# Kernel optimization log

Measured on AMD Instinct MI355X. Metric: run time of the kernel, lower is better.

The kernel has to match this reference:

```python
import jax, jax.numpy as jnp
import numpy as np

N = 100000   # nodes (single ntype)
R = 3        # relations
E = 500000   # edges per relation
H = 4        # attention heads
F = 64       # out_feat per head
IN = 256     # in_feat
NEG_SLOPE = 0.2  # DGL GATConv default


def setup_inputs() -> dict:
    key = jax.random.key(0)
    ks = jax.random.split(key, 7)
    x = jax.random.normal(ks[0], (N, IN), jnp.float32)
    src = jax.random.randint(ks[1], (R, E), 0, N, dtype=jnp.int32)
    dst = jax.random.randint(ks[2], (R, E), 0, N, dtype=jnp.int32)
    W = jax.random.normal(ks[3], (R, IN, H * F), jnp.float32) / np.sqrt(IN).astype(np.float32)
    attn_l = jax.random.normal(ks[4], (R, H, F), jnp.float32) * 0.1
    attn_r = jax.random.normal(ks[5], (R, H, F), jnp.float32) * 0.1
    bias = jnp.zeros((R, H * F), jnp.float32)
    return {"x": x, "W": W, "attn_l": attn_l, "attn_r": attn_r, "bias": bias,
            "src": src, "dst": dst}


def _gat_relation(x, W_r, al_r, ar_r, b_r, src_r, dst_r):
    # projection: [N, H, F]
    z = (x @ W_r).reshape(N, H, F)
    # per-node attention logits: [N, H]
    el = jnp.sum(z * al_r, axis=-1)
    er = jnp.sum(z * ar_r, axis=-1)
    # edge scores: [E, H]
    e = jax.nn.leaky_relu(el[src_r] + er[dst_r], negative_slope=NEG_SLOPE)
    # segment softmax over incoming edges of each dst node
    m = jax.ops.segment_max(e, dst_r, num_segments=N)      # [N, H]
    ee = jnp.exp(e - m[dst_r])                              # [E, H]
    den = jax.ops.segment_sum(ee, dst_r, num_segments=N)   # [N, H]
    alpha = ee / den[dst_r]                                 # [E, H]
    # weighted scatter-aggregate: [N, H, F]
    rst = jax.ops.segment_sum(z[src_r] * alpha[:, :, None], dst_r, num_segments=N)
    return rst + b_r.reshape(1, H, F)


def reference(x, W, attn_l, attn_r, bias, src, dst):
    # HeteroGraphConv aggregates relations targeting the same ntype with 'sum'
    out = jnp.zeros((N, H, F), x.dtype)
    for r in range(R):
        out = out + _gat_relation(x, W[r], attn_l[r], attn_r[r], bias[r], src[r], dst[r])
    # RelGATConvLayer._apply: activation(h.view(-1, out_feat*num_heads)); dropout=0
    return jax.nn.elu(out.reshape(N, H * F))
```

## Files before the change

### kernel.cpp

```cpp
#include <hip/hip_runtime.h>
#include <hip/hip_bf16.h>


#define RN 100000
#define RE 500000
#define RH 4
#define RIN 256
#define RR 3
#define RHF 256
#define NE3 (RR * RE)
#define N3  (RR * RN)

typedef __attribute__((ext_vector_type(8))) short short8;
typedef __attribute__((ext_vector_type(4))) float f32x4;

static __device__ __forceinline__ float b2f(unsigned short u) {
  return __uint_as_float(((unsigned int)u) << 16);
}
static __device__ __forceinline__ unsigned short f2b(float f) {
  unsigned int u = __float_as_uint(f);
  u += 0x7FFF + ((u >> 16) & 1);
  return (unsigned short)(u >> 16);
}
static __device__ __forceinline__ float h2f(unsigned short u) {
  return (float)__builtin_bit_cast(_Float16, u);
}
static __device__ __forceinline__ unsigned short f2h(float f) {
  return __builtin_bit_cast(unsigned short, (_Float16)f);
}
static __device__ __forceinline__ unsigned int cvt_pk_bf16(float lo, float hi) {
  unsigned int r;
  asm("v_cvt_pk_bf16_f32 %0, %1, %2" : "=v"(r) : "v"(lo), "v"(hi));
  return r;
}

__global__ __launch_bounds__(256) void rgat_convx(
    const float* __restrict__ x, unsigned short* __restrict__ xb) {
  const size_t i = ((size_t)blockIdx.x * 256 + threadIdx.x) * 4;
  if (i >= (size_t)RN * RIN) return;
  const float4 v = *(const float4*)(x + i);
  ushort4 o;
  o.x = f2b(v.x); o.y = f2b(v.y); o.z = f2b(v.z); o.w = f2b(v.w);
  *(ushort4*)(xb + i) = o;
}

__global__ __launch_bounds__(256) void rgat_convw(
    const float* __restrict__ W, unsigned short* __restrict__ wbt) {
  const int o = blockIdx.x * 256 + threadIdx.x;
  if (o >= RR * RIN * RHF) return;
  const int r = o / (RIN * RHF);
  const int rem = o - r * (RIN * RHF);
  const int n = rem >> 8;
  const int k = rem & 255;
  wbt[o] = f2b(W[r * (RIN * RHF) + k * RHF + n]);
}

__global__ __launch_bounds__(256) void rgat_gemm_bf16(
    const unsigned short* __restrict__ xb, const unsigned short* __restrict__ wbt,
    unsigned short* __restrict__ zb, const float* __restrict__ al,
    const float* __restrict__ ar, unsigned short* __restrict__ elh,
    unsigned short* __restrict__ erh) {
  __shared__ unsigned short As[128 * 32];
  __shared__ unsigned short Bs[128 * 32];
  const int tid = threadIdx.x;
  const int lane = tid & 63, wid = tid >> 6;
  const int wr = wid >> 1, wc = wid & 1;
  const int m0 = blockIdx.x * 128;
  const int n0 = blockIdx.y * 128;
  const int r  = blockIdx.z;

  f32x4 acc[4][4] = {};
  const unsigned short* Bbase = wbt + (size_t)r * (RIN * RHF);

  for (int k0 = 0; k0 < RIN; k0 += 32) {
#pragma unroll
    for (int i = 0; i < 2; ++i) {
      const int c = wid * 128 + i * 64 + lane;
      const int row = c >> 2, c4 = c & 3;
      const unsigned short* ga = xb + (size_t)(m0 + row) * RIN + k0 + c4 * 8;
      __builtin_amdgcn_global_load_lds(
          (const __attribute__((address_space(1))) void*)ga,
          (__attribute__((address_space(3))) void*)(As + (wid * 128 + i * 64) * 8),
          16, 0, 0);
      const unsigned short* gb = Bbase + (size_t)(n0 + row) * RIN + k0 + c4 * 8;
      __builtin_amdgcn_global_load_lds(
          (const __attribute__((address_space(1))) void*)gb,
          (__attribute__((address_space(3))) void*)(Bs + (wid * 128 + i * 64) * 8),
          16, 0, 0);
    }
    asm volatile("s_waitcnt vmcnt(0)" ::: "memory");
    __syncthreads();

    short8 wf[4], xf[4];
#pragma unroll
    for (int ci = 0; ci < 4; ++ci)
      wf[ci] = *(const short8*)(Bs + ((wr * 64 + ci * 16 + (lane & 15)) * 32 + (lane >> 4) * 8));
#pragma unroll
    for (int xi = 0; xi < 4; ++xi)
      xf[xi] = *(const short8*)(As + ((wc * 64 + xi * 16 + (lane & 15)) * 32 + (lane >> 4) * 8));
#pragma unroll
    for (int ci = 0; ci < 4; ++ci)
#pragma unroll
      for (int xi = 0; xi < 4; ++xi)
        acc[ci][xi] = __builtin_amdgcn_mfma_f32_16x16x32_bf16(wf[ci], xf[xi], acc[ci][xi], 0, 0, 0);
    __syncthreads();
  }

  const int head = blockIdx.y * 2 + wr;
  const int g4 = (lane >> 4) * 4;
  float alv[4][4], arv[4][4];
#pragma unroll
  for (int ci = 0; ci < 4; ++ci) {
    const float4 a4 = *(const float4*)(al + r * RHF + head * 64 + ci * 16 + g4);
    const float4 b4 = *(const float4*)(ar + r * RHF + head * 64 + ci * 16 + g4);
    alv[ci][0] = a4.x; alv[ci][1] = a4.y; alv[ci][2] = a4.z; alv[ci][3] = a4.w;
    arv[ci][0] = b4.x; arv[ci][1] = b4.y; arv[ci][2] = b4.z; arv[ci][3] = b4.w;
  }

#pragma unroll
  for (int xi = 0; xi < 4; ++xi) {
    const int node = m0 + wc * 64 + xi * 16 + (lane & 15);
    unsigned short* zrow = zb + (size_t)r * ((size_t)RN * RHF) + (size_t)node * RHF
                           + n0 + wr * 64 + g4;
    float pl = 0.f, pr = 0.f;
#pragma unroll
    for (int ci = 0; ci < 4; ++ci) {
      const f32x4 a = acc[ci][xi];
      uint2 pk;
      pk.x = cvt_pk_bf16(a[0], a[1]);
      pk.y = cvt_pk_bf16(a[2], a[3]);
      if (node < RN) *(uint2*)(zrow + ci * 16) = pk;
      pl += a[0] * alv[ci][0] + a[1] * alv[ci][1] + a[2] * alv[ci][2] + a[3] * alv[ci][3];
      pr += a[0] * arv[ci][0] + a[1] * arv[ci][1] + a[2] * arv[ci][2] + a[3] * arv[ci][3];
    }
    pl += __shfl_xor(pl, 16); pl += __shfl_xor(pl, 32);
    pr += __shfl_xor(pr, 16); pr += __shfl_xor(pr, 32);
    if (lane < 16 && node < RN) {
      const size_t key = (size_t)r * RN + node;
      elh[key * RH + head] = f2h(pl);
      erh[key * RH + head] = f2h(pr);
    }
  }
}

__global__ __launch_bounds__(256) void rgat_hist(
    const int* __restrict__ dst, int* __restrict__ deg2) {
  const int i = blockIdx.x * 256 + threadIdx.x;
  if (i >= NE3) return;
  const int r = i / RE;
  atomicAdd(&deg2[dst[i] * RR + r], 1);
}

__global__ __launch_bounds__(256) void rgat_scan1(
    const int* __restrict__ deg, int* __restrict__ offs, int* __restrict__ bsum) {
  __shared__ int sh[256];
  const int tid = threadIdx.x;
  const int base = blockIdx.x * 1024 + tid * 4;
  int v[4]; int s = 0;
#pragma unroll
  for (int j = 0; j < 4; ++j) {
    v[j] = (base + j < N3) ? deg[base + j] : 0;
    s += v[j];
  }
  sh[tid] = s;
  __syncthreads();
  for (int off = 1; off < 256; off <<= 1) {
    int t = (tid >= off) ? sh[tid - off] : 0;
    __syncthreads();
    sh[tid] += t;
    __syncthreads();
  }
  int run = sh[tid] - s;
  if (tid == 255) bsum[blockIdx.x] = sh[255];
#pragma unroll
  for (int j = 0; j < 4; ++j) {
    if (base + j < N3) offs[base + j] = run;
    run += v[j];
  }
}

__global__ __launch_bounds__(512) void rgat_scan2(int* __restrict__ bsum, int nb) {
  __shared__ int sh[512];
  const int tid = threadIdx.x;
  const int v = (tid < nb) ? bsum[tid] : 0;
  sh[tid] = v;
  __syncthreads();
  for (int off = 1; off < 512; off <<= 1) {
    int t = (tid >= off) ? sh[tid - off] : 0;
    __syncthreads();
    sh[tid] += t;
    __syncthreads();
  }
  if (tid < nb) bsum[tid] = sh[tid] - v;
}

__global__ __launch_bounds__(256) void rgat_scan3(
    int* __restrict__ offs, const int* __restrict__ bsum) {
  const int base = blockIdx.x * 1024 + threadIdx.x * 4;
  const int b = bsum[blockIdx.x];
#pragma unroll
  for (int j = 0; j < 4; ++j)
    if (base + j < N3) offs[base + j] += b;
}

__global__ __launch_bounds__(256) void rgat_scatter(
    const int* __restrict__ src, const int* __restrict__ dst,
    const unsigned short* __restrict__ elh, const unsigned short* __restrict__ erh,
    int* __restrict__ offs2, int* __restrict__ czoff,
    unsigned short* __restrict__ ceeh) {
  const int i = blockIdx.x * 256 + threadIdx.x;
  if (i >= NE3) return;
  const int r = i / RE;
  const int s = src[i];
  const int d = dst[i];
  const int pos = atomicAdd(&offs2[d * RR + r], 1);
  const uint2 eu = *(const uint2*)(elh + ((size_t)r * RN + s) * RH);
  const uint2 ru = *(const uint2*)(erh + ((size_t)r * RN + d) * RH);
  float e0 = h2f((unsigned short)eu.x) + h2f((unsigned short)ru.x);
  float e1 = h2f((unsigned short)(eu.x >> 16)) + h2f((unsigned short)(ru.x >> 16));
  float e2 = h2f((unsigned short)eu.y) + h2f((unsigned short)ru.y);
  float e3 = h2f((unsigned short)(eu.y >> 16)) + h2f((unsigned short)(ru.y >> 16));
  e0 = e0 > 0.f ? e0 : 0.2f * e0;
  e1 = e1 > 0.f ? e1 : 0.2f * e1;
  e2 = e2 > 0.f ? e2 : 0.2f * e2;
  e3 = e3 > 0.f ? e3 : 0.2f * e3;
  czoff[pos] = r * RN + s;
  uint2 o;
  o.x = (unsigned int)f2h(__expf(e0)) | ((unsigned int)f2h(__expf(e1)) << 16);
  o.y = (unsigned int)f2h(__expf(e2)) | ((unsigned int)f2h(__expf(e3)) << 16);
  *(uint2*)(ceeh + (size_t)pos * 4) = o;
}

__global__ __launch_bounds__(256) void rgat_norm(
    unsigned short* __restrict__ ceeh, const int* __restrict__ deg2,
    const int* __restrict__ offs2) {
  const int key = blockIdx.x * 256 + threadIdx.x;
  if (key >= N3) return;
  const int d = deg2[key];
  const int end = offs2[key];
  float s0 = 0.f, s1 = 0.f, s2 = 0.f, s3 = 0.f;
  for (int p = end - d; p < end; ++p) {
    const uint2 v = *(const uint2*)(ceeh + (size_t)p * 4);
    s0 += h2f((unsigned short)v.x);
    s1 += h2f((unsigned short)(v.x >> 16));
    s2 += h2f((unsigned short)v.y);
    s3 += h2f((unsigned short)(v.y >> 16));
  }
  const float i0 = s0 > 0.f ? 1.f / s0 : 0.f;
  const float i1 = s1 > 0.f ? 1.f / s1 : 0.f;
  const float i2 = s2 > 0.f ? 1.f / s2 : 0.f;
  const float i3 = s3 > 0.f ? 1.f / s3 : 0.f;
  for (int p = end - d; p < end; ++p) {
    uint2 v = *(const uint2*)(ceeh + (size_t)p * 4);
    const float a0 = h2f((unsigned short)v.x) * i0;
    const float a1 = h2f((unsigned short)(v.x >> 16)) * i1;
    const float a2 = h2f((unsigned short)v.y) * i2;
    const float a3 = h2f((unsigned short)(v.y >> 16)) * i3;
    v.x = (unsigned int)f2h(a0) | ((unsigned int)f2h(a1) << 16);
    v.y = (unsigned int)f2h(a2) | ((unsigned int)f2h(a3) << 16);
    *(uint2*)(ceeh + (size_t)p * 4) = v;
  }
}

__global__ __launch_bounds__(256) void rgat_aggregate(
    const unsigned short* __restrict__ zb, const int* __restrict__ czoff,
    const unsigned short* __restrict__ ceeh, const int* __restrict__ deg2,
    const int* __restrict__ offs2, const float* __restrict__ bias,
    float* __restrict__ out) {
  __shared__ float shn[4][RHF];
  const int n = blockIdx.x;
  const int tid = threadIdx.x;
  const int wid = tid >> 6, lane = tid & 63;
  const int hw = lane >> 5;
  const int sub = lane & 31;
  const int hwid = wid * 2 + hw;
  const int h = sub >> 3;
  const int c = sub * 8;

  const int k0 = n * RR;
  const int start = offs2[k0] - deg2[k0];
  const int dm = offs2[k0 + 2] - start;

  float acc[8] = {};
  const unsigned short* zB = zb + c;

  for (int base = 0; base < dm; base += 16) {
    int ss[2]; float aa[2];
#pragma unroll
    for (int j = 0; j < 2; ++j) {
      const int t = base + j * 8 + hwid;
      const int tc = t < dm ? t : dm - 1;
      const int p = start + tc;
      ss[j] = czoff[p];
      const float af = h2f(ceeh[(size_t)p * 4 + h]);
      aa[j] = t < dm ? af : 0.f;
    }
    short8 zv[2];
#pragma unroll
    for (int j = 0; j < 2; ++j)
      zv[j] = *(const short8*)(zB + (size_t)ss[j] * RHF);
#pragma unroll
    for (int j = 0; j < 2; ++j) {
      const float a = aa[j];
#pragma unroll
      for (int k = 0; k < 8; ++k)
        acc[k] += a * b2f((unsigned short)zv[j][k]);
    }
  }

#pragma unroll
  for (int k = 0; k < 8; ++k) acc[k] += __shfl_xor(acc[k], 32);

  if (lane < 32) {
    *(float4*)&shn[wid][c]     = make_float4(acc[0], acc[1], acc[2], acc[3]);
    *(float4*)&shn[wid][c + 4] = make_float4(acc[4], acc[5], acc[6], acc[7]);
  }
  __syncthreads();

  const int col = tid;
  float v = shn[0][col] + shn[1][col] + shn[2][col] + shn[3][col]
          + bias[col] + bias[RHF + col] + bias[2 * RHF + col];
  v = v > 0.f ? v : (__expf(v) - 1.f);
  out[(size_t)n * RHF + col] = v;
}

extern "C" void kernel_launch(void* const* d_in, const int* in_sizes, int n_in,
                              void* d_out, int out_size, void* d_ws, size_t ws_size,
                              hipStream_t stream) {
  const float* x    = (const float*)d_in[0];
  const float* W    = (const float*)d_in[1];
  const float* al   = (const float*)d_in[2];
  const float* ar   = (const float*)d_in[3];
  const float* bias = (const float*)d_in[4];
  const int*   src  = (const int*)d_in[5];
  const int*   dst  = (const int*)d_in[6];
  float* out = (float*)d_out;

  char* p = (char*)d_ws;
  unsigned short* xb   = (unsigned short*)p; p += (size_t)RN * RIN * 2;
  unsigned short* wbt  = (unsigned short*)p; p += (size_t)RR * RIN * RHF * 2;
  unsigned short* zb   = (unsigned short*)p; p += (size_t)RR * RN * RHF * 2;
  unsigned short* elh  = (unsigned short*)p; p += (size_t)N3 * RH * 2;
  unsigned short* erh  = (unsigned short*)p; p += (size_t)N3 * RH * 2;
  int* deg2    = (int*)p;    p += (size_t)N3 * 4;
  int* offs2   = (int*)p;    p += (size_t)N3 * 4;
  int* czoff   = (int*)p;    p += (size_t)NE3 * 4;
  unsigned short* ceeh = (unsigned short*)p; p += (size_t)NE3 * RH * 2;
  int* bsum    = (int*)p;    p += 2048;

  const int NB1 = (N3 + 1023) / 1024;

  hipMemsetAsync(deg2, 0, (size_t)N3 * 4, stream);

  rgat_convx<<<(RN * RIN / 4 + 255) / 256, 256, 0, stream>>>(x, xb);
  rgat_convw<<<(RR * RIN * RHF + 255) / 256, 256, 0, stream>>>(W, wbt);

  rgat_hist<<<(NE3 + 255) / 256, 256, 0, stream>>>(dst, deg2);
  rgat_scan1<<<NB1, 256, 0, stream>>>(deg2, offs2, bsum);
  rgat_scan2<<<1, 512, 0, stream>>>(bsum, NB1);
  rgat_scan3<<<NB1, 256, 0, stream>>>(offs2, bsum);

  rgat_gemm_bf16<<<dim3((RN + 127) / 128, RHF / 128, RR), 256, 0, stream>>>(
      xb, wbt, zb, al, ar, elh, erh);

  rgat_scatter<<<(NE3 + 255) / 256, 256, 0, stream>>>(src, dst, elh, erh, offs2,
                                                      czoff, ceeh);

  rgat_norm<<<(N3 + 255) / 256, 256, 0, stream>>>(ceeh, deg2, offs2);

  rgat_aggregate<<<RN, 256, 0, stream>>>(zb, czoff, ceeh, deg2, offs2, bias, out);
}
```

Before: 603.5 us.

## Widen GEMM tile to full 256 columns and move edge score computation into norm

The GEMM block now covers all 256 output columns (all four heads) per 128-node tile, so each block loads the x tile once instead of twice. It drops the grid's column dimension, doubles the B shared buffer and per-thread accumulators, which raises register pressure. Edge logit and exp computation moves from the atomic scatter kernel into the per-destination norm kernel. There it reuses the destination's er value and the CSR source offsets, and the sum is taken in fp32 before fp16 rounding, so scatter no longer writes the ceeh buffer.

```diff
diff --git a/kernel.cpp b/kernel.cpp
--- a/kernel.cpp
+++ b/kernel.cpp
@@ -61,52 +61,53 @@
     const float* __restrict__ ar, unsigned short* __restrict__ elh,
     unsigned short* __restrict__ erh) {
   __shared__ unsigned short As[128 * 32];
-  __shared__ unsigned short Bs[128 * 32];
+  __shared__ unsigned short Bs[256 * 32];
   const int tid = threadIdx.x;
   const int lane = tid & 63, wid = tid >> 6;
-  const int wr = wid >> 1, wc = wid & 1;
   const int m0 = blockIdx.x * 128;
-  const int n0 = blockIdx.y * 128;
-  const int r  = blockIdx.z;
-
-  f32x4 acc[4][4] = {};
+  const int r  = blockIdx.y;
+
+  f32x4 acc[4][8] = {};
   const unsigned short* Bbase = wbt + (size_t)r * (RIN * RHF);
 
   for (int k0 = 0; k0 < RIN; k0 += 32) {
 #pragma unroll
     for (int i = 0; i < 2; ++i) {
-      const int c = wid * 128 + i * 64 + lane;
+      const int c = i * 256 + tid;
       const int row = c >> 2, c4 = c & 3;
       const unsigned short* ga = xb + (size_t)(m0 + row) * RIN + k0 + c4 * 8;
       __builtin_amdgcn_global_load_lds(
           (const __attribute__((address_space(1))) void*)ga,
-          (__attribute__((address_space(3))) void*)(As + (wid * 128 + i * 64) * 8),
-          16, 0, 0);
-      const unsigned short* gb = Bbase + (size_t)(n0 + row) * RIN + k0 + c4 * 8;
+          (__attribute__((address_space(3))) void*)(As + c * 8), 16, 0, 0);
+    }
+#pragma unroll
+    for (int i = 0; i < 4; ++i) {
+      const int c = i * 256 + tid;
+      const int row = c >> 2, c4 = c & 3;
+      const unsigned short* gb = Bbase + (size_t)row * RIN + k0 + c4 * 8;
       __builtin_amdgcn_global_load_lds(
           (const __attribute__((address_space(1))) void*)gb,
-          (__attribute__((address_space(3))) void*)(Bs + (wid * 128 + i * 64) * 8),
-          16, 0, 0);
+          (__attribute__((address_space(3))) void*)(Bs + c * 8), 16, 0, 0);
     }
     asm volatile("s_waitcnt vmcnt(0)" ::: "memory");
     __syncthreads();
 
-    short8 wf[4], xf[4];
+    short8 wf[4], xf[8];
 #pragma unroll
     for (int ci = 0; ci < 4; ++ci)
-      wf[ci] = *(const short8*)(Bs + ((wr * 64 + ci * 16 + (lane & 15)) * 32 + (lane >> 4) * 8));
-#pragma unroll
-    for (int xi = 0; xi < 4; ++xi)
-      xf[xi] = *(const short8*)(As + ((wc * 64 + xi * 16 + (lane & 15)) * 32 + (lane >> 4) * 8));
+      wf[ci] = *(const short8*)(Bs + ((wid * 64 + ci * 16 + (lane & 15)) * 32 + (lane >> 4) * 8));
+#pragma unroll
+    for (int xi = 0; xi < 8; ++xi)
+      xf[xi] = *(const short8*)(As + ((xi * 16 + (lane & 15)) * 32 + (lane >> 4) * 8));
 #pragma unroll
     for (int ci = 0; ci < 4; ++ci)
 #pragma unroll
-      for (int xi = 0; xi < 4; ++xi)
+      for (int xi = 0; xi < 8; ++xi)
         acc[ci][xi] = __builtin_amdgcn_mfma_f32_16x16x32_bf16(wf[ci], xf[xi], acc[ci][xi], 0, 0, 0);
     __syncthreads();
   }
 
-  const int head = blockIdx.y * 2 + wr;
+  const int head = wid;
   const int g4 = (lane >> 4) * 4;
   float alv[4][4], arv[4][4];
 #pragma unroll
@@ -118,10 +119,10 @@
   }
 
 #pragma unroll
-  for (int xi = 0; xi < 4; ++xi) {
-    const int node = m0 + wc * 64 + xi * 16 + (lane & 15);
+  for (int xi = 0; xi < 8; ++xi) {
+    const int node = m0 + xi * 16 + (lane & 15);
     unsigned short* zrow = zb + (size_t)r * ((size_t)RN * RHF) + (size_t)node * RHF
-                           + n0 + wr * 64 + g4;
+                           + head * 64 + g4;
     float pl = 0.f, pr = 0.f;
 #pragma unroll
     for (int ci = 0; ci < 4; ++ci) {
@@ -205,46 +206,48 @@
 
 __global__ __launch_bounds__(256) void rgat_scatter(
     const int* __restrict__ src, const int* __restrict__ dst,
-    const unsigned short* __restrict__ elh, const unsigned short* __restrict__ erh,
-    int* __restrict__ offs2, int* __restrict__ czoff,
-    unsigned short* __restrict__ ceeh) {
+    int* __restrict__ offs2, int* __restrict__ czoff) {
   const int i = blockIdx.x * 256 + threadIdx.x;
   if (i >= NE3) return;
   const int r = i / RE;
   const int s = src[i];
   const int d = dst[i];
   const int pos = atomicAdd(&offs2[d * RR + r], 1);
-  const uint2 eu = *(const uint2*)(elh + ((size_t)r * RN + s) * RH);
-  const uint2 ru = *(const uint2*)(erh + ((size_t)r * RN + d) * RH);
-  float e0 = h2f((unsigned short)eu.x) + h2f((unsigned short)ru.x);
-  float e1 = h2f((unsigned short)(eu.x >> 16)) + h2f((unsigned short)(ru.x >> 16));
-  float e2 = h2f((unsigned short)eu.y) + h2f((unsigned short)ru.y);
-  float e3 = h2f((unsigned short)(eu.y >> 16)) + h2f((unsigned short)(ru.y >> 16));
-  e0 = e0 > 0.f ? e0 : 0.2f * e0;
-  e1 = e1 > 0.f ? e1 : 0.2f * e1;
-  e2 = e2 > 0.f ? e2 : 0.2f * e2;
-  e3 = e3 > 0.f ? e3 : 0.2f * e3;
   czoff[pos] = r * RN + s;
-  uint2 o;
-  o.x = (unsigned int)f2h(__expf(e0)) | ((unsigned int)f2h(__expf(e1)) << 16);
-  o.y = (unsigned int)f2h(__expf(e2)) | ((unsigned int)f2h(__expf(e3)) << 16);
-  *(uint2*)(ceeh + (size_t)pos * 4) = o;
 }
 
 __global__ __launch_bounds__(256) void rgat_norm(
-    unsigned short* __restrict__ ceeh, const int* __restrict__ deg2,
-    const int* __restrict__ offs2) {
+    const int* __restrict__ czoff, const unsigned short* __restrict__ elh,
+    const unsigned short* __restrict__ erh, const int* __restrict__ deg2,
+    const int* __restrict__ offs2, unsigned short* __restrict__ ceeh) {
   const int key = blockIdx.x * 256 + threadIdx.x;
   if (key >= N3) return;
   const int d = deg2[key];
+  if (d == 0) return;
   const int end = offs2[key];
+  const int r = key % RR;
+  const int dnode = key / RR;
+  const uint2 ru = *(const uint2*)(erh + ((size_t)r * RN + dnode) * RH);
+  const float er0 = h2f((unsigned short)ru.x), er1 = h2f((unsigned short)(ru.x >> 16));
+  const float er2 = h2f((unsigned short)ru.y), er3 = h2f((unsigned short)(ru.y >> 16));
   float s0 = 0.f, s1 = 0.f, s2 = 0.f, s3 = 0.f;
   for (int p = end - d; p < end; ++p) {
-    const uint2 v = *(const uint2*)(ceeh + (size_t)p * 4);
-    s0 += h2f((unsigned short)v.x);
-    s1 += h2f((unsigned short)(v.x >> 16));
-    s2 += h2f((unsigned short)v.y);
-    s3 += h2f((unsigned short)(v.y >> 16));
+    const int zo = czoff[p];
+    const uint2 eu = *(const uint2*)(elh + (size_t)zo * RH);
+    float e0 = h2f((unsigned short)eu.x) + er0;
+    float e1 = h2f((unsigned short)(eu.x >> 16)) + er1;
+    float e2 = h2f((unsigned short)eu.y) + er2;
+    float e3 = h2f((unsigned short)(eu.y >> 16)) + er3;
+    e0 = e0 > 0.f ? e0 : 0.2f * e0;
+    e1 = e1 > 0.f ? e1 : 0.2f * e1;
+    e2 = e2 > 0.f ? e2 : 0.2f * e2;
+    e3 = e3 > 0.f ? e3 : 0.2f * e3;
+    const float p0 = __expf(e0), p1 = __expf(e1), p2 = __expf(e2), p3 = __expf(e3);
+    s0 += p0; s1 += p1; s2 += p2; s3 += p3;
+    uint2 o;
+    o.x = (unsigned int)f2h(p0) | ((unsigned int)f2h(p1) << 16);
+    o.y = (unsigned int)f2h(p2) | ((unsigned int)f2h(p3) << 16);
+    *(uint2*)(ceeh + (size_t)p * 4) = o;
   }
   const float i0 = s0 > 0.f ? 1.f / s0 : 0.f;
   const float i1 = s1 > 0.f ? 1.f / s1 : 0.f;
@@ -360,13 +363,12 @@
   rgat_scan2<<<1, 512, 0, stream>>>(bsum, NB1);
   rgat_scan3<<<NB1, 256, 0, stream>>>(offs2, bsum);
 
-  rgat_gemm_bf16<<<dim3((RN + 127) / 128, RHF / 128, RR), 256, 0, stream>>>(
+  rgat_gemm_bf16<<<dim3((RN + 127) / 128, RR), 256, 0, stream>>>(
       xb, wbt, zb, al, ar, elh, erh);
 
-  rgat_scatter<<<(NE3 + 255) / 256, 256, 0, stream>>>(src, dst, elh, erh, offs2,
-                                                      czoff, ceeh);
-
-  rgat_norm<<<(N3 + 255) / 256, 256, 0, stream>>>(ceeh, deg2, offs2);
+  rgat_scatter<<<(NE3 + 255) / 256, 256, 0, stream>>>(src, dst, offs2, czoff);
+
+  rgat_norm<<<(N3 + 255) / 256, 256, 0, stream>>>(czoff, elh, erh, deg2, offs2, ceeh);
 
   rgat_aggregate<<<RN, 256, 0, stream>>>(zb, czoff, ceeh, deg2, offs2, bias, out);
 }
```

Measured after the change: 661.4 us. 1.1x slower.

## Merge prep kernels into one launch and widen GEMM tile to full N

Applied to the files above, without the earlier changes.

Fuses the x conversion, W transpose-conversion and degree histogram into a single kernel dispatched by block index, removing two launches. The GEMM now computes all 256 output columns per block (one head per wave, 128x256 tile), so each x tile is read once instead of twice. The cost is doubled accumulator registers (32 f32x4 per thread) and larger shared memory, which may lower occupancy.

```diff
diff --git a/kernel.cpp b/kernel.cpp
--- a/kernel.cpp
+++ b/kernel.cpp
@@ -11,6 +11,10 @@
 #define NE3 (RR * RE)
 #define N3  (RR * RN)
 
+#define CVX_BLOCKS ((RN * RIN / 4 + 255) / 256)
+#define CVW_BLOCKS ((RR * RIN * RHF + 255) / 256)
+#define HIST_BLOCKS ((NE3 + 255) / 256)
+
 typedef __attribute__((ext_vector_type(8))) short short8;
 typedef __attribute__((ext_vector_type(4))) float f32x4;
 
@@ -34,25 +38,32 @@
   return r;
 }
 
-__global__ __launch_bounds__(256) void rgat_convx(
-    const float* __restrict__ x, unsigned short* __restrict__ xb) {
-  const size_t i = ((size_t)blockIdx.x * 256 + threadIdx.x) * 4;
-  if (i >= (size_t)RN * RIN) return;
-  const float4 v = *(const float4*)(x + i);
-  ushort4 o;
-  o.x = f2b(v.x); o.y = f2b(v.y); o.z = f2b(v.z); o.w = f2b(v.w);
-  *(ushort4*)(xb + i) = o;
-}
-
-__global__ __launch_bounds__(256) void rgat_convw(
-    const float* __restrict__ W, unsigned short* __restrict__ wbt) {
-  const int o = blockIdx.x * 256 + threadIdx.x;
-  if (o >= RR * RIN * RHF) return;
-  const int r = o / (RIN * RHF);
-  const int rem = o - r * (RIN * RHF);
-  const int n = rem >> 8;
-  const int k = rem & 255;
-  wbt[o] = f2b(W[r * (RIN * RHF) + k * RHF + n]);
+__global__ __launch_bounds__(256) void rgat_prep(
+    const float* __restrict__ x, unsigned short* __restrict__ xb,
+    const float* __restrict__ W, unsigned short* __restrict__ wbt,
+    const int* __restrict__ dst, int* __restrict__ deg2) {
+  const int b = blockIdx.x;
+  if (b < CVX_BLOCKS) {
+    const size_t i = ((size_t)b * 256 + threadIdx.x) * 4;
+    if (i >= (size_t)RN * RIN) return;
+    const float4 v = *(const float4*)(x + i);
+    ushort4 o;
+    o.x = f2b(v.x); o.y = f2b(v.y); o.z = f2b(v.z); o.w = f2b(v.w);
+    *(ushort4*)(xb + i) = o;
+  } else if (b < CVX_BLOCKS + CVW_BLOCKS) {
+    const int o = (b - CVX_BLOCKS) * 256 + threadIdx.x;
+    if (o >= RR * RIN * RHF) return;
+    const int r = o / (RIN * RHF);
+    const int rem = o - r * (RIN * RHF);
+    const int n = rem >> 8;
+    const int k = rem & 255;
+    wbt[o] = f2b(W[r * (RIN * RHF) + k * RHF + n]);
+  } else {
+    const int i = (b - CVX_BLOCKS - CVW_BLOCKS) * 256 + threadIdx.x;
+    if (i >= NE3) return;
+    const int r = i / RE;
+    atomicAdd(&deg2[dst[i] * RR + r], 1);
+  }
 }
 
 __global__ __launch_bounds__(256) void rgat_gemm_bf16(
@@ -61,52 +72,53 @@
     const float* __restrict__ ar, unsigned short* __restrict__ elh,
     unsigned short* __restrict__ erh) {
   __shared__ unsigned short As[128 * 32];
-  __shared__ unsigned short Bs[128 * 32];
+  __shared__ unsigned short Bs[256 * 32];
   const int tid = threadIdx.x;
   const int lane = tid & 63, wid = tid >> 6;
-  const int wr = wid >> 1, wc = wid & 1;
   const int m0 = blockIdx.x * 128;
-  const int n0 = blockIdx.y * 128;
-  const int r  = blockIdx.z;
-
-  f32x4 acc[4][4] = {};
+  const int r  = blockIdx.y;
+
+  f32x4 acc[4][8] = {};
   const unsigned short* Bbase = wbt + (size_t)r * (RIN * RHF);
 
   for (int k0 = 0; k0 < RIN; k0 += 32) {
 #pragma unroll
     for (int i = 0; i < 2; ++i) {
-      const int c = wid * 128 + i * 64 + lane;
+      const int c = i * 256 + tid;
       const int row = c >> 2, c4 = c & 3;
       const unsigned short* ga = xb + (size_t)(m0 + row) * RIN + k0 + c4 * 8;
       __builtin_amdgcn_global_load_lds(
           (const __attribute__((address_space(1))) void*)ga,
-          (__attribute__((address_space(3))) void*)(As + (wid * 128 + i * 64) * 8),
-          16, 0, 0);
-      const unsigned short* gb = Bbase + (size_t)(n0 + row) * RIN + k0 + c4 * 8;
+          (__attribute__((address_space(3))) void*)(As + c * 8), 16, 0, 0);
+    }
+#pragma unroll
+    for (int i = 0; i < 4; ++i) {
+      const int c = i * 256 + tid;
+      const int row = c >> 2, c4 = c & 3;
+      const unsigned short* gb = Bbase + (size_t)row * RIN + k0 + c4 * 8;
       __builtin_amdgcn_global_load_lds(
           (const __attribute__((address_space(1))) void*)gb,
-          (__attribute__((address_space(3))) void*)(Bs + (wid * 128 + i * 64) * 8),
-          16, 0, 0);
+          (__attribute__((address_space(3))) void*)(Bs + c * 8), 16, 0, 0);
     }
     asm volatile("s_waitcnt vmcnt(0)" ::: "memory");
     __syncthreads();
 
-    short8 wf[4], xf[4];
+    short8 wf[4], xf[8];
 #pragma unroll
     for (int ci = 0; ci < 4; ++ci)
-      wf[ci] = *(const short8*)(Bs + ((wr * 64 + ci * 16 + (lane & 15)) * 32 + (lane >> 4) * 8));
-#pragma unroll
-    for (int xi = 0; xi < 4; ++xi)
-      xf[xi] = *(const short8*)(As + ((wc * 64 + xi * 16 + (lane & 15)) * 32 + (lane >> 4) * 8));
+      wf[ci] = *(const short8*)(Bs + ((wid * 64 + ci * 16 + (lane & 15)) * 32 + (lane >> 4) * 8));
+#pragma unroll
+    for (int xi = 0; xi < 8; ++xi)
+      xf[xi] = *(const short8*)(As + ((xi * 16 + (lane & 15)) * 32 + (lane >> 4) * 8));
 #pragma unroll
     for (int ci = 0; ci < 4; ++ci)
 #pragma unroll
-      for (int xi = 0; xi < 4; ++xi)
+      for (int xi = 0; xi < 8; ++xi)
         acc[ci][xi] = __builtin_amdgcn_mfma_f32_16x16x32_bf16(wf[ci], xf[xi], acc[ci][xi], 0, 0, 0);
     __syncthreads();
   }
 
-  const int head = blockIdx.y * 2 + wr;
+  const int head = wid;
   const int g4 = (lane >> 4) * 4;
   float alv[4][4], arv[4][4];
 #pragma unroll
@@ -118,10 +130,10 @@
   }
 
 #pragma unroll
-  for (int xi = 0; xi < 4; ++xi) {
-    const int node = m0 + wc * 64 + xi * 16 + (lane & 15);
+  for (int xi = 0; xi < 8; ++xi) {
+    const int node = m0 + xi * 16 + (lane & 15);
     unsigned short* zrow = zb + (size_t)r * ((size_t)RN * RHF) + (size_t)node * RHF
-                           + n0 + wr * 64 + g4;
+                           + head * 64 + g4;
     float pl = 0.f, pr = 0.f;
 #pragma unroll
     for (int ci = 0; ci < 4; ++ci) {
@@ -141,14 +153,6 @@
       erh[key * RH + head] = f2h(pr);
     }
   }
-}
-
-__global__ __launch_bounds__(256) void rgat_hist(
-    const int* __restrict__ dst, int* __restrict__ deg2) {
-  const int i = blockIdx.x * 256 + threadIdx.x;
-  if (i >= NE3) return;
-  const int r = i / RE;
-  atomicAdd(&deg2[dst[i] * RR + r], 1);
 }
 
 __global__ __launch_bounds__(256) void rgat_scan1(
@@ -352,15 +356,14 @@
 
   hipMemsetAsync(deg2, 0, (size_t)N3 * 4, stream);
 
-  rgat_convx<<<(RN * RIN / 4 + 255) / 256, 256, 0, stream>>>(x, xb);
-  rgat_convw<<<(RR * RIN * RHF + 255) / 256, 256, 0, stream>>>(W, wbt);
-
-  rgat_hist<<<(NE3 + 255) / 256, 256, 0, stream>>>(dst, deg2);
+  rgat_prep<<<CVX_BLOCKS + CVW_BLOCKS + HIST_BLOCKS, 256, 0, stream>>>(
+      x, xb, W, wbt, dst, deg2);
+
   rgat_scan1<<<NB1, 256, 0, stream>>>(deg2, offs2, bsum);
   rgat_scan2<<<1, 512, 0, stream>>>(bsum, NB1);
   rgat_scan3<<<NB1, 256, 0, stream>>>(offs2, bsum);
 
-  rgat_gemm_bf16<<<dim3((RN + 127) / 128, RHF / 128, RR), 256, 0, stream>>>(
+  rgat_gemm_bf16<<<dim3((RN + 127) / 128, RR), 256, 0, stream>>>(
       xb, wbt, zb, al, ar, elh, erh);
 
   rgat_scatter<<<(NE3 + 255) / 256, 256, 0, stream>>>(src, dst, elh, erh, offs2,
```

Measured after the change: 618.5 us. 1.02x slower.
